# Optimization experiments

Measured on AMD Instinct MI355X. Metric: run time of the kernel, lower is better.

The kernel has to match this reference:

```python
import jax, jax.numpy as jnp
import numpy as np

THETA = 1.0
V_TH = 1.0       # spikingjelly IFNode default v_threshold
SG_ALPHA = 4.0   # spikingjelly surrogate.Sigmoid default alpha


@jax.custom_vjp
def heaviside(x):
    # spike = 1 if membrane - threshold >= 0
    return (x >= 0).astype(x.dtype)

def _heaviside_fwd(x):
    return (x >= 0).astype(x.dtype), x

def _heaviside_bwd(x, g):
    s = jax.nn.sigmoid(SG_ALPHA * x)
    return (g * SG_ALPHA * s * (1.0 - s),)

heaviside.defvjp(_heaviside_fwd, _heaviside_bwd)


@jax.custom_vjp
def spike_aggregate(spike_out, z_total):
    return spike_out

def _sa_fwd(spike_out, z_total):
    return spike_out, z_total

def _sa_bwd(z_total, g):
    surrogate = (z_total > 0).astype(g.dtype) / THETA
    return (jnp.zeros_like(g), g * surrogate)

spike_aggregate.defvjp(_sa_fwd, _sa_bwd)


def setup_inputs() -> dict:
    key = jax.random.key(0)
    k_x, k_w1, k_b1, k_w2, k_b2 = jax.random.split(key, 5)
    B, D_in, H, D_out = 4096, 784, 800, 10
    x = jax.random.uniform(k_x, (B, D_in), dtype=jnp.float32)
    # nn.Linear-style init: U(-1/sqrt(fan_in), 1/sqrt(fan_in))
    s1 = 1.0 / np.sqrt(D_in)
    s2 = 1.0 / np.sqrt(H)
    W1 = jax.random.uniform(k_w1, (H, D_in), jnp.float32, -s1, s1)
    b1 = jax.random.uniform(k_b1, (H,), jnp.float32, -s1, s1)
    W2 = jax.random.uniform(k_w2, (D_out, H), jnp.float32, -s2, s2)
    b2 = jax.random.uniform(k_b2, (D_out,), jnp.float32, -s2, s2)
    return {"x": x, "W1": W1, "b1": b1, "W2": W2, "b2": b2, "T_sim": 32}


def reference(x, W1, b1, W2, b2, T_sim):
    B = x.shape[0]
    x = x.reshape(B, -1)
    # fixed Bernoulli rate encoding (rand_like(x) < x)
    u = jax.random.uniform(jax.random.key(42), x.shape, dtype=x.dtype)
    x_fixed = (u < x).astype(x.dtype)
    # fc1 input is the same every timestep -> compute once
    cur1 = x_fixed @ W1.T + b1                     # [B, 800]

    def step(carry, _):
        v1, v2, count, z_total = carry
        h1 = v1 + cur1
        spk1 = heaviside(h1 - V_TH)
        v1 = h1 * (1.0 - jax.lax.stop_gradient(spk1))  # hard reset to 0, detach_reset
        cur2 = spk1 @ W2.T + b2                    # [B, 10]
        z_total = z_total + cur2
        h2 = v2 + cur2
        spk2 = heaviside(h2 - V_TH)
        v2 = h2 * (1.0 - jax.lax.stop_gradient(spk2))
        count = count + spk2
        return (v1, v2, count, z_total), None

    H, D_out = W1.shape[0], W2.shape[0]
    init = (jnp.zeros((B, H), x.dtype), jnp.zeros((B, D_out), x.dtype),
            jnp.zeros((B, D_out), x.dtype), jnp.zeros((B, D_out), x.dtype))
    (v1, v2, count, z_total), _ = jax.lax.scan(step, init, None, length=T_sim)
    return spike_aggregate(count, z_total)
```

## Files before the change

kernel.cpp:

```cpp
#include <hip/hip_runtime.h>
#include <stdint.h>

#define B_ROWS 4096
#define D_IN   784
#define H_DIM  800
#define D_OUT  10
#define T_SIM  32
#define N_ELEM (B_ROWS * D_IN)
#define CAP    512
#define R_PER  2

__device__ __forceinline__ void threefry2x32(uint32_t k0, uint32_t k1,
                                             uint32_t& x0, uint32_t& x1) {
  uint32_t ks0 = k0, ks1 = k1, ks2 = k0 ^ k1 ^ 0x1BD11BDAu;
  x0 += ks0; x1 += ks1;
#define TF_RND(r) { x0 += x1; x1 = (x1 << (r)) | (x1 >> (32 - (r))); x1 ^= x0; }
  TF_RND(13) TF_RND(15) TF_RND(26) TF_RND(6)
  x0 += ks1; x1 += ks2 + 1u;
  TF_RND(17) TF_RND(29) TF_RND(16) TF_RND(24)
  x0 += ks2; x1 += ks0 + 2u;
  TF_RND(13) TF_RND(15) TF_RND(26) TF_RND(6)
  x0 += ks0; x1 += ks1 + 3u;
  TF_RND(17) TF_RND(29) TF_RND(16) TF_RND(24)
  x0 += ks1; x1 += ks2 + 4u;
  TF_RND(13) TF_RND(15) TF_RND(26) TF_RND(6)
  x0 += ks2; x1 += ks0 + 5u;
#undef TF_RND
}

__global__ __launch_bounds__(256) void gen_xfixed(const float* __restrict__ x,
                                                  float* __restrict__ xf) {
  int i = blockIdx.x * blockDim.x + threadIdx.x;
  if (i >= N_ELEM) return;
  uint32_t c0 = 0u, c1 = (uint32_t)i;
  threefry2x32(0u, 42u, c0, c1);
  uint32_t bits = c0 ^ c1;
  float u = __uint_as_float((bits >> 9) | 0x3F800000u) - 1.0f;
  xf[i] = (u < x[i]) ? 1.0f : 0.0f;
}

#define BM 128
#define BN 64
#define BK 16

__global__ __launch_bounds__(256) void gemm_cur1(const float* __restrict__ xf,
                                                 const float* __restrict__ W1,
                                                 const float* __restrict__ b1,
                                                 float* __restrict__ cur1) {
  __shared__ __align__(16) float As[BK][BM + 4];
  __shared__ __align__(16) float Bs[BK][BN + 4];
  const int m0 = blockIdx.y * BM;
  const int n0 = blockIdx.x * BN;
  const int t  = threadIdx.x;
  const int tx = t & 15, ty = t >> 4;
  const int ar = t >> 1;
  const int ak = (t & 1) * 8;
  const int br = t >> 2;
  const int bk = (t & 3) * 4;
  const int hB = n0 + br;
  const bool bOK = (hB < H_DIM);
  const float* aptr = xf + (m0 + ar) * D_IN + ak;
  const float* bptr = W1 + (bOK ? hB : 0) * D_IN + bk;

  float4 a0 = *(const float4*)(aptr);
  float4 a1 = *(const float4*)(aptr + 4);
  float4 b0 = *(const float4*)(bptr);
  if (!bOK) { b0.x = b0.y = b0.z = b0.w = 0.0f; }

  float acc[8][4] = {};
  for (int kt = 0; kt < D_IN; kt += BK) {
    As[ak + 0][ar] = a0.x; As[ak + 1][ar] = a0.y;
    As[ak + 2][ar] = a0.z; As[ak + 3][ar] = a0.w;
    As[ak + 4][ar] = a1.x; As[ak + 5][ar] = a1.y;
    As[ak + 6][ar] = a1.z; As[ak + 7][ar] = a1.w;
    Bs[bk + 0][br] = b0.x; Bs[bk + 1][br] = b0.y;
    Bs[bk + 2][br] = b0.z; Bs[bk + 3][br] = b0.w;
    __syncthreads();
    if (kt + BK < D_IN) {
      a0 = *(const float4*)(aptr + kt + BK);
      a1 = *(const float4*)(aptr + kt + BK + 4);
      b0 = *(const float4*)(bptr + kt + BK);
      if (!bOK) { b0.x = b0.y = b0.z = b0.w = 0.0f; }
    }
#pragma unroll
    for (int kk = 0; kk < BK; kk++) {
      float4 av0 = *(const float4*)&As[kk][ty * 8];
      float4 av1 = *(const float4*)&As[kk][ty * 8 + 4];
      float4 bv  = *(const float4*)&Bs[kk][tx * 4];
      float a[8] = {av0.x, av0.y, av0.z, av0.w, av1.x, av1.y, av1.z, av1.w};
      float b[4] = {bv.x, bv.y, bv.z, bv.w};
#pragma unroll
      for (int mi = 0; mi < 8; mi++)
#pragma unroll
        for (int ni = 0; ni < 4; ni++)
          acc[mi][ni] = __builtin_fmaf(a[mi], b[ni], acc[mi][ni]);
    }
    __syncthreads();
  }
  const int hOut = n0 + tx * 4;
  if (hOut < H_DIM) {
    float4 bb = *(const float4*)&b1[hOut];
#pragma unroll
    for (int mi = 0; mi < 8; mi++) {
      int m = m0 + ty * 8 + mi;
      float4 r;
      r.x = acc[mi][0] + bb.x;
      r.y = acc[mi][1] + bb.y;
      r.z = acc[mi][2] + bb.z;
      r.w = acc[mi][3] + bb.w;
      *(float4*)&cur1[m * H_DIM + hOut] = r;
    }
  }
}

__global__ __launch_bounds__(320) void snn_scan(const float* __restrict__ cur1,
                                                const float* __restrict__ W2,
                                                const float* __restrict__ b2,
                                                float* __restrict__ out) {
  __shared__ uint8_t  per_s[R_PER][832];
  __shared__ uint16_t hidx[R_PER][CAP];
  __shared__ uint32_t mks[R_PER][CAP];
  __shared__ __align__(16) float wv[R_PER][CAP][D_OUT];
  __shared__ int      lenL[R_PER];
  __shared__ uint32_t divm_s[T_SIM];
  __shared__ float    c2s[R_PER][T_SIM][D_OUT];
  __shared__ float    b2f[D_OUT];
  const int tid  = threadIdx.x;
  const int row0 = blockIdx.x * R_PER;

  if (tid < D_OUT) b2f[tid] = b2[tid];
  if (tid < T_SIM) {
    uint32_t dm = 0;
#pragma unroll
    for (int p = 1; p <= T_SIM; p++)
      if ((tid + 1) % p == 0) dm |= 1u << (p - 1);
    divm_s[tid] = dm;
  }

  for (int e = tid; e < R_PER * 832; e += 320) {
    int r = (e >= 832) ? 1 : 0;
    int h = e - r * 832;
    int p = 0;
    if (h < H_DIM) {
      float c = cur1[(size_t)(row0 + r) * H_DIM + h];
      float v = 0.0f;
#pragma unroll 1
      for (int m = 1; m <= T_SIM; m++) {
        float h1 = v + c;
        if (h1 >= 1.0f) { p = m; break; }
        v = h1;
      }
    }
    per_s[r][h] = (uint8_t)p;
  }
  __syncthreads();

  if (tid < 128) {
    const int r = tid >> 6, ln = tid & 63;
    const uint64_t lmask = (1ull << ln) - 1ull;
    int off = 0;
    for (int ch = 0; ch < 13; ch++) {
      int h = ch * 64 + ln;
      int p = per_s[r][h];
      bool g = (p != 0);
      uint64_t bal = __ballot(g);
      int pos = off + __popcll(bal & lmask);
      if (g && pos < CAP) {
        hidx[r][pos] = (uint16_t)h;
        uint32_t mk = 0;
        for (int s = p; s <= T_SIM; s += p) mk |= 1u << (s - 1);
        mks[r][pos] = mk;
      }
      off += __popcll(bal);
    }
    if (ln == 0) lenL[r] = off;
  }
  __syncthreads();

  {
    const int L0 = min(lenL[0], CAP), L1 = min(lenL[1], CAP);
    for (int e = tid; e < R_PER * CAP; e += 320) {
      int r = e >> 9, i = e & (CAP - 1);
      int Lr = r ? L1 : L0;
      if (i >= Lr) {
        mks[r][i] = 0u;
      } else {
        int h = hidx[r][i];
#pragma unroll
        for (int o = 0; o < D_OUT; o++)
          wv[r][i][o] = W2[o * H_DIM + h];
      }
    }
  }
  __syncthreads();

  {
    const int t = tid & 31, r = (tid >> 5) & 1, j = tid >> 6;
    const int Lr = lenL[r];
    float s0 = 0.0f, s1 = 0.0f;
    if (Lr <= CAP) {
      const int Lmax = max(min(lenL[0], CAP), min(lenL[1], CAP));
      const uint32_t* mp = mks[r];
      const float*    wp = &wv[r][0][2 * j];
#pragma unroll 4
      for (int i = 0; i < Lmax; i++) {
        uint32_t mk = mp[i];
        float2 w = *(const float2*)wp; wp += D_OUT;
        bool g = (mk >> t) & 1u;
        s0 += g ? w.x : 0.0f;
        s1 += g ? w.y : 0.0f;
      }
    } else {
      const uint32_t dm = divm_s[t];
      for (int h = 0; h < H_DIM; h++) {
        int p = per_s[r][h];
        bool g = p && ((dm >> (p - 1)) & 1u);
        float w0 = W2[(2 * j) * H_DIM + h];
        float w1 = W2[(2 * j + 1) * H_DIM + h];
        s0 += g ? w0 : 0.0f;
        s1 += g ? w1 : 0.0f;
      }
    }
    c2s[r][t][2 * j]     = s0;
    c2s[r][t][2 * j + 1] = s1;
  }
  __syncthreads();

  if (tid < R_PER * D_OUT) {
    const int r = tid / D_OUT, o = tid % D_OUT;
    const float bb = b2f[o];
    float v = 0.0f; int cnt = 0;
#pragma unroll
    for (int t = 0; t < T_SIM; t++) {
      float cur2 = c2s[r][t][o] + bb;
      float h2 = v + cur2;
      bool spk = (h2 >= 1.0f);
      cnt += spk ? 1 : 0;
      v = spk ? 0.0f : h2;
    }
    out[(size_t)(row0 + r) * D_OUT + o] = (float)cnt;
  }
}

extern "C" void kernel_launch(void* const* d_in, const int* in_sizes, int n_in,
                              void* d_out, int out_size, void* d_ws, size_t ws_size,
                              hipStream_t stream) {
  const float* x  = (const float*)d_in[0];
  const float* W1 = (const float*)d_in[1];
  const float* b1 = (const float*)d_in[2];
  const float* W2 = (const float*)d_in[3];
  const float* b2 = (const float*)d_in[4];
  float* outp = (float*)d_out;

  float* xf   = (float*)d_ws;
  float* cur1 = xf + N_ELEM;

  gen_xfixed<<<N_ELEM / 256, 256, 0, stream>>>(x, xf);

  dim3 g1((H_DIM + BN - 1) / BN, B_ROWS / BM);
  gemm_cur1<<<g1, 256, 0, stream>>>(xf, W1, b1, cur1);

  snn_scan<<<B_ROWS / R_PER, 320, 0, stream>>>(cur1, W2, b2, outp);
}
```

Baseline: 331.1 us.

## Fuse spike-period computation into GEMM epilogue and stage transposed W2 in LDS

The GEMM epilogue now computes each hidden neuron's first-spike period and writes it as one byte per element, instead of writing the fp32 cur1 matrix. This cuts the intermediate write and read traffic by a factor of four. The scan kernel loads W2 transposed into shared memory once per block and indexes it through byte offsets, replacing the per-row gather of W2 columns. It also uses a precomputed period-to-mask table and a smaller CAP. In exchange, each block redundantly loads all of W2 (32 KB), and the period loop now runs serially in the GEMM threads.

```diff
diff --git a/kernel.cpp b/kernel.cpp
--- a/kernel.cpp
+++ b/kernel.cpp
@@ -7,7 +7,7 @@
 #define D_OUT  10
 #define T_SIM  32
 #define N_ELEM (B_ROWS * D_IN)
-#define CAP    512
+#define CAP    448
 #define R_PER  2
 
 __device__ __forceinline__ void threefry2x32(uint32_t k0, uint32_t k1,
@@ -43,10 +43,10 @@
 #define BN 64
 #define BK 16
 
-__global__ __launch_bounds__(256) void gemm_cur1(const float* __restrict__ xf,
-                                                 const float* __restrict__ W1,
-                                                 const float* __restrict__ b1,
-                                                 float* __restrict__ cur1) {
+__global__ __launch_bounds__(256) void gemm_periods(const float* __restrict__ xf,
+                                                    const float* __restrict__ W1,
+                                                    const float* __restrict__ b1,
+                                                    uint8_t* __restrict__ pb) {
   __shared__ __align__(16) float As[BK][BM + 4];
   __shared__ __align__(16) float Bs[BK][BN + 4];
   const int m0 = blockIdx.y * BM;
@@ -103,122 +103,116 @@
 #pragma unroll
     for (int mi = 0; mi < 8; mi++) {
       int m = m0 + ty * 8 + mi;
-      float4 r;
-      r.x = acc[mi][0] + bb.x;
-      r.y = acc[mi][1] + bb.y;
-      r.z = acc[mi][2] + bb.z;
-      r.w = acc[mi][3] + bb.w;
-      *(float4*)&cur1[m * H_DIM + hOut] = r;
-    }
-  }
-}
-
-__global__ __launch_bounds__(320) void snn_scan(const float* __restrict__ cur1,
+      float c4[4];
+      c4[0] = acc[mi][0] + bb.x;
+      c4[1] = acc[mi][1] + bb.y;
+      c4[2] = acc[mi][2] + bb.z;
+      c4[3] = acc[mi][3] + bb.w;
+      uint32_t packed = 0;
+#pragma unroll
+      for (int ni = 0; ni < 4; ni++) {
+        float c = c4[ni];
+        float v = 0.0f;
+        int p = 0;
+#pragma unroll 1
+        for (int s = 1; s <= T_SIM; s++) {
+          float h1 = v + c;
+          if (h1 >= 1.0f) { p = s; break; }
+          v = h1;
+        }
+        packed |= (uint32_t)p << (8 * ni);
+      }
+      *(uint32_t*)&pb[(size_t)m * H_DIM + hOut] = packed;
+    }
+  }
+}
+
+__global__ __launch_bounds__(320) void snn_scan(const uint8_t* __restrict__ pb,
                                                 const float* __restrict__ W2,
                                                 const float* __restrict__ b2,
                                                 float* __restrict__ out) {
-  __shared__ uint8_t  per_s[R_PER][832];
-  __shared__ uint16_t hidx[R_PER][CAP];
+  __shared__ __align__(16) float W2T[H_DIM * D_OUT];
+  __shared__ uint16_t ha16[R_PER][CAP];
   __shared__ uint32_t mks[R_PER][CAP];
-  __shared__ __align__(16) float wv[R_PER][CAP][D_OUT];
   __shared__ int      lenL[R_PER];
-  __shared__ uint32_t divm_s[T_SIM];
+  __shared__ uint32_t mask_tbl[T_SIM + 1];
   __shared__ float    c2s[R_PER][T_SIM][D_OUT];
   __shared__ float    b2f[D_OUT];
   const int tid  = threadIdx.x;
   const int row0 = blockIdx.x * R_PER;
 
   if (tid < D_OUT) b2f[tid] = b2[tid];
-  if (tid < T_SIM) {
-    uint32_t dm = 0;
-#pragma unroll
-    for (int p = 1; p <= T_SIM; p++)
-      if ((tid + 1) % p == 0) dm |= 1u << (p - 1);
-    divm_s[tid] = dm;
-  }
-
-  for (int e = tid; e < R_PER * 832; e += 320) {
-    int r = (e >= 832) ? 1 : 0;
-    int h = e - r * 832;
-    int p = 0;
-    if (h < H_DIM) {
-      float c = cur1[(size_t)(row0 + r) * H_DIM + h];
-      float v = 0.0f;
-#pragma unroll 1
-      for (int m = 1; m <= T_SIM; m++) {
-        float h1 = v + c;
-        if (h1 >= 1.0f) { p = m; break; }
-        v = h1;
-      }
-    }
-    per_s[r][h] = (uint8_t)p;
+  if (tid <= T_SIM) {
+    uint32_t mk = 0;
+    if (tid > 0) for (int s = tid; s <= T_SIM; s += tid) mk |= 1u << (s - 1);
+    mask_tbl[tid] = mk;
   }
   __syncthreads();
 
   if (tid < 128) {
     const int r = tid >> 6, ln = tid & 63;
     const uint64_t lmask = (1ull << ln) - 1ull;
-    int off = 0;
+    uint8_t pv[13];
+#pragma unroll
     for (int ch = 0; ch < 13; ch++) {
       int h = ch * 64 + ln;
-      int p = per_s[r][h];
+      pv[ch] = (h < H_DIM) ? pb[(size_t)(row0 + r) * H_DIM + h] : (uint8_t)0;
+    }
+    int off = 0;
+#pragma unroll
+    for (int ch = 0; ch < 13; ch++) {
+      int h = ch * 64 + ln;
+      int p = pv[ch];
       bool g = (p != 0);
       uint64_t bal = __ballot(g);
       int pos = off + __popcll(bal & lmask);
       if (g && pos < CAP) {
-        hidx[r][pos] = (uint16_t)h;
-        uint32_t mk = 0;
-        for (int s = p; s <= T_SIM; s += p) mk |= 1u << (s - 1);
-        mks[r][pos] = mk;
+        ha16[r][pos] = (uint16_t)(h * 40);
+        mks[r][pos]  = mask_tbl[p];
       }
       off += __popcll(bal);
     }
     if (ln == 0) lenL[r] = off;
-  }
-  __syncthreads();
-
-  {
-    const int L0 = min(lenL[0], CAP), L1 = min(lenL[1], CAP);
-    for (int e = tid; e < R_PER * CAP; e += 320) {
-      int r = e >> 9, i = e & (CAP - 1);
-      int Lr = r ? L1 : L0;
-      if (i >= Lr) {
-        mks[r][i] = 0u;
-      } else {
-        int h = hidx[r][i];
-#pragma unroll
-        for (int o = 0; o < D_OUT; o++)
-          wv[r][i][o] = W2[o * H_DIM + h];
-      }
-    }
+  } else {
+    for (int e = tid - 128; e < H_DIM * D_OUT; e += 192) {
+      int o = e / H_DIM, h = e - o * H_DIM;
+      W2T[h * D_OUT + o] = W2[e];
+    }
+  }
+  __syncthreads();
+
+  const int L0 = min(lenL[0], CAP), L1 = min(lenL[1], CAP);
+  for (int e = tid; e < R_PER * CAP; e += 320) {
+    int r = e / CAP, i = e - r * CAP;
+    if (i >= (r ? L1 : L0)) { mks[r][i] = 0u; ha16[r][i] = 0; }
   }
   __syncthreads();
 
   {
     const int t = tid & 31, r = (tid >> 5) & 1, j = tid >> 6;
-    const int Lr = lenL[r];
     float s0 = 0.0f, s1 = 0.0f;
-    if (Lr <= CAP) {
-      const int Lmax = max(min(lenL[0], CAP), min(lenL[1], CAP));
+    if (lenL[0] <= CAP && lenL[1] <= CAP) {
+      const int Lmax = max(L0, L1);
+      const uint16_t* hp = ha16[r];
       const uint32_t* mp = mks[r];
-      const float*    wp = &wv[r][0][2 * j];
-#pragma unroll 4
+      const float*    wbase = W2T + 2 * j;
+#pragma unroll 8
       for (int i = 0; i < Lmax; i++) {
+        uint32_t ha = hp[i];
         uint32_t mk = mp[i];
-        float2 w = *(const float2*)wp; wp += D_OUT;
+        float2 w = *(const float2*)((const char*)wbase + ha);
         bool g = (mk >> t) & 1u;
         s0 += g ? w.x : 0.0f;
         s1 += g ? w.y : 0.0f;
       }
     } else {
-      const uint32_t dm = divm_s[t];
+      const uint8_t* prow = pb + (size_t)(row0 + r) * H_DIM;
       for (int h = 0; h < H_DIM; h++) {
-        int p = per_s[r][h];
-        bool g = p && ((dm >> (p - 1)) & 1u);
-        float w0 = W2[(2 * j) * H_DIM + h];
-        float w1 = W2[(2 * j + 1) * H_DIM + h];
-        s0 += g ? w0 : 0.0f;
-        s1 += g ? w1 : 0.0f;
+        uint32_t mk = mask_tbl[prow[h]];
+        float2 w = *(const float2*)&W2T[h * D_OUT + 2 * j];
+        bool g = (mk >> t) & 1u;
+        s0 += g ? w.x : 0.0f;
+        s1 += g ? w.y : 0.0f;
       }
     }
     c2s[r][t][2 * j]     = s0;
@@ -252,13 +246,13 @@
   const float* b2 = (const float*)d_in[4];
   float* outp = (float*)d_out;
 
-  float* xf   = (float*)d_ws;
-  float* cur1 = xf + N_ELEM;
+  float*   xf = (float*)d_ws;
+  uint8_t* pbuf = (uint8_t*)(xf + N_ELEM);
 
   gen_xfixed<<<N_ELEM / 256, 256, 0, stream>>>(x, xf);
 
   dim3 g1((H_DIM + BN - 1) / BN, B_ROWS / BM);
-  gemm_cur1<<<g1, 256, 0, stream>>>(xf, W1, b1, cur1);
-
-  snn_scan<<<B_ROWS / R_PER, 320, 0, stream>>>(cur1, W2, b2, outp);
-}
+  gemm_periods<<<g1, 256, 0, stream>>>(xf, W1, b1, pbuf);
+
+  snn_scan<<<B_ROWS / R_PER, 320, 0, stream>>>(pbuf, W2, b2, outp);
+}
```

Result: faster. 296.8 us (-10.4%).
